# Kernel optimization log

Measured on AMD Instinct MI355X. Metric: run time of the kernel, lower is better.

## Reference

```python
import jax, jax.numpy as jnp
import numpy as np

EPS = 1e-08

def setup_inputs() -> dict:
    key = jax.random.key(0)
    kH, kF, kQ, kK, kV = jax.random.split(key, 5)
    B, N, d = 8192, 16, 512
    H = jax.random.normal(kH, (B, N, d), dtype=jnp.float32)
    F_raw = jax.random.uniform(kF, (B, N), dtype=jnp.float32)
    F = F_raw / jnp.sum(F_raw, axis=-1, keepdims=True)  # fractions sum to 1
    s = 1.0 / np.sqrt(d)
    W_Q = jax.random.normal(kQ, (d, d), dtype=jnp.float32) * s
    W_K = jax.random.normal(kK, (d, d), dtype=jnp.float32) * s
    W_V = jax.random.normal(kV, (d, d), dtype=jnp.float32) * s
    return {"H": H, "F": F, "W_Q": W_Q, "W_K": W_K, "W_V": W_V}

def reference(H, F, W_Q, W_K, W_V):
    d = H.shape[-1]
    scale = jnp.asarray(d, H.dtype) ** 0.5
    # nn.Linear(d, d, bias=False): y = x @ W.T
    Q = jnp.einsum('bnd,ed->bne', H, W_Q)
    K = jnp.einsum('bnd,ed->bne', H, W_K)
    V = jnp.einsum('bnd,ed->bne', H, W_V)
    scores = jnp.einsum('bqd,bkd->bqk', Q, K) / scale  # [B,N,N]
    scores = scores + jnp.log(F + EPS)[:, None, :]      # fraction bias over keys
    alpha = jax.nn.softmax(scores, axis=-1)
    h_attn = jnp.einsum('bqk,bkd->bqd', alpha, V)
    h_out = H + h_attn                                  # residual
    h_poly = jnp.einsum('bn,bnd->bd', F, h_out)         # fraction-weighted pool
    return h_poly
```

## Files before the change

### kernel.cpp

```cpp
#include <hip/hip_runtime.h>

typedef __bf16 bf16x8 __attribute__((ext_vector_type(8)));
typedef float f32x4 __attribute__((ext_vector_type(4)));

__device__ __forceinline__ unsigned short f2bf(float f) {
    unsigned int u = __builtin_bit_cast(unsigned int, f);
    u += 0x7fffu + ((u >> 16) & 1u);
    return (unsigned short)(u >> 16);
}
__device__ __forceinline__ float bf2f(unsigned short u) {
    return __builtin_bit_cast(float, (unsigned)u << 16);
}

__device__ __forceinline__ unsigned swz1k(unsigned byte) {
    return byte ^ ((byte >> 6) & 0x70u);
}

__device__ __forceinline__ void bar_lgkm() {
    asm volatile("s_waitcnt lgkmcnt(0)\n\ts_barrier" ::: "memory");
}
#define SB() __builtin_amdgcn_sched_barrier(0)

__global__ __launch_bounds__(256) void prep_kernel(
    const float* __restrict__ Wq, const float* __restrict__ Wk,
    const float* __restrict__ Wv, unsigned short* __restrict__ Pc,
    unsigned short* __restrict__ Wvb)
{
    int b = blockIdx.x;
    if (b < 1024) {
        int j0 = (b >> 4) * 8;
        int kc = b & 15;
        int jloc = threadIdx.x >> 5;
        int t = threadIdx.x & 31;
        int j = j0 + jloc, d = kc * 32 + t;
        float acc = 0.f;
        #pragma unroll 8
        for (int e = 0; e < 512; ++e)
            acc = fmaf(Wk[e * 512 + j], Wq[e * 512 + d], acc);
        Pc[((kc * 512) + j) * 32 + t] = f2bf(acc);
    } else {
        int i = (b - 1024) * 256 + (int)threadIdx.x;
        Wvb[i] = f2bf(Wv[i]);
    }
}

__device__ __forceinline__ void issue_q(int q, int tid, const float4* hsrc, float4 (&hq)[2]) {
    #pragma unroll
    for (int r = 0; r < 2; ++r) {
        int flat = r * 1024 + tid;
        hq[r] = hsrc[(flat >> 5) * 128 + q * 32 + (flat & 31)];
    }
}

__device__ __forceinline__ void convert_q(int q, int tid, char* HBF, float4 (&hq)[2]) {
    #pragma unroll
    for (int r = 0; r < 2; ++r) {
        int flat = r * 1024 + tid;
        int row = flat >> 5, ch = flat & 31;
        ushort4 bv;
        bv.x = f2bf(hq[r].x); bv.y = f2bf(hq[r].y);
        bv.z = f2bf(hq[r].z); bv.w = f2bf(hq[r].w);
        *(ushort4*)(HBF + swz1k((unsigned)row * 1024u + (unsigned)(q * 32 + ch) * 8u)) = bv;
    }
}

template<bool PREF>
__device__ __forceinline__ void gemm_q(
    int kcbase, int tid, int rl, int kg,
    const unsigned short* bptr, char* HBF,
    bf16x8 (&st0)[2], bf16x8 (&st1)[2],
    f32x4 (&acc)[4][2],
    float4 (&hq)[2], const float4* hsrc, int hq_q)
{
    #pragma unroll
    for (int k = 0; k < 4; ++k) {
        const int kc = kcbase + k;
        bf16x8 bn[2];
        if (kc + 2 < 16) {
            #pragma unroll
            for (int jj = 0; jj < 2; ++jj)
                bn[jj] = *(const bf16x8*)(bptr + (kc + 2) * 16384 + jj * 512);
        }
        if (PREF && k == 1) {
            SB();
            issue_q(hq_q, tid, hsrc, hq);
            SB();
        }
        bf16x8 a[4];
        #pragma unroll
        for (int i = 0; i < 4; ++i) {
            unsigned off = (unsigned)(i * 16 + rl) * 1024u + (unsigned)kc * 64u + (unsigned)kg * 16u;
            a[i] = *(bf16x8*)(HBF + swz1k(off));
        }
        #pragma unroll
        for (int i = 0; i < 4; ++i)
            #pragma unroll
            for (int jj = 0; jj < 2; ++jj)
                acc[i][jj] = __builtin_amdgcn_mfma_f32_16x16x32_bf16(a[i], st0[jj], acc[i][jj], 0, 0, 0);
        #pragma unroll
        for (int jj = 0; jj < 2; ++jj) { st0[jj] = st1[jj]; st1[jj] = bn[jj]; }
    }
}

__global__ __launch_bounds__(1024, 4) void attn_main_kernel(
    const float* __restrict__ H, const float* __restrict__ F,
    const unsigned short* __restrict__ Pc,
    float* __restrict__ out, unsigned short* __restrict__ g_ws)
{
    extern __shared__ char smem[];
    char* HBF  = smem;
    char* TBF  = smem + 65536;
    float* wbuf = (float*)(smem + 131072);
    float* FL   = (float*)(smem + 131328);
    float* LFL  = (float*)(smem + 131584);

    const int tid = threadIdx.x;
    const int wv = tid >> 6;
    const int ln = tid & 63;
    const int rl = ln & 15;
    const int kg = ln >> 4;
    const int blk = blockIdx.x;
    const long long gr0 = (long long)blk * 64;
    const float4* hsrc = (const float4*)(H + gr0 * 512);

    float fval = 0.f;
    if (tid < 64) fval = F[blk * 64 + tid];

    float4 hqA[2], hqB[2];
    issue_q(0, tid, hsrc, hqA);

    const unsigned short* bptr = Pc + ((wv * 32 + rl) * 32 + kg * 8);
    bf16x8 st0[2], st1[2];
    #pragma unroll
    for (int jj = 0; jj < 2; ++jj) st0[jj] = *(const bf16x8*)(bptr + 0 * 16384 + jj * 512);
    #pragma unroll
    for (int jj = 0; jj < 2; ++jj) st1[jj] = *(const bf16x8*)(bptr + 1 * 16384 + jj * 512);

    issue_q(1, tid, hsrc, hqB);

    if (tid < 64) {
        FL[tid] = fval;
        LFL[tid] = logf(fval + 1e-8f);
    }

    f32x4 acc[4][2];
    #pragma unroll
    for (int i = 0; i < 4; ++i)
        #pragma unroll
        for (int jj = 0; jj < 2; ++jj)
            acc[i][jj] = f32x4{0.f, 0.f, 0.f, 0.f};

    convert_q(0, tid, HBF, hqA);
    bar_lgkm();
    gemm_q<true >(0,  tid, rl, kg, bptr, HBF, st0, st1, acc, hqA, hsrc, 2);
    convert_q(1, tid, HBF, hqB);
    bar_lgkm();
    gemm_q<true >(4,  tid, rl, kg, bptr, HBF, st0, st1, acc, hqB, hsrc, 3);
    convert_q(2, tid, HBF, hqA);
    bar_lgkm();
    gemm_q<false>(8,  tid, rl, kg, bptr, HBF, st0, st1, acc, hqA, hsrc, 0);
    convert_q(3, tid, HBF, hqB);
    bar_lgkm();
    gemm_q<false>(12, tid, rl, kg, bptr, HBF, st0, st1, acc, hqB, hsrc, 0);

    #pragma unroll
    for (int i = 0; i < 4; ++i)
        #pragma unroll
        for (int jj = 0; jj < 2; ++jj)
            #pragma unroll
            for (int p = 0; p < 4; ++p) {
                unsigned row = (unsigned)(i * 16 + kg * 4 + p);
                unsigned col = (unsigned)(wv * 32 + jj * 16 + rl);
                *(unsigned short*)(TBF + swz1k(row * 1024u + col * 2u)) = f2bf(acc[i][jj][p]);
            }
    bar_lgkm();

    if (wv < 4) {
        f32x4 sc0 = f32x4{0.f,0.f,0.f,0.f}, sc1 = sc0, sc2 = sc0, sc3 = sc0;
        __builtin_amdgcn_s_setprio(1);
        #pragma unroll
        for (int kc = 0; kc < 16; ++kc) {
            unsigned off = (unsigned)(wv * 16 + rl) * 1024u + (unsigned)kc * 64u + (unsigned)kg * 16u;
            bf16x8 aT = *(bf16x8*)(TBF + swz1k(off));
            bf16x8 bH = *(bf16x8*)(HBF + swz1k(off));
            if ((kc & 3) == 0) sc0 = __builtin_amdgcn_mfma_f32_16x16x32_bf16(aT, bH, sc0, 0, 0, 0);
            else if ((kc & 3) == 1) sc1 = __builtin_amdgcn_mfma_f32_16x16x32_bf16(aT, bH, sc1, 0, 0, 0);
            else if ((kc & 3) == 2) sc2 = __builtin_amdgcn_mfma_f32_16x16x32_bf16(aT, bH, sc2, 0, 0, 0);
            else sc3 = __builtin_amdgcn_mfma_f32_16x16x32_bf16(aT, bH, sc3, 0, 0, 0);
        }
        __builtin_amdgcn_s_setprio(0);
        f32x4 sc;
        #pragma unroll
        for (int p = 0; p < 4; ++p) sc[p] = (sc0[p] + sc1[p]) + (sc2[p] + sc3[p]);

        float bias = LFL[wv * 16 + rl];
        float alpha[4];
        #pragma unroll
        for (int p = 0; p < 4; ++p) {
            float s = sc[p] * 0.044194173824159216f + bias;
            float m = s;
            m = fmaxf(m, __shfl_xor(m, 8));
            m = fmaxf(m, __shfl_xor(m, 4));
            m = fmaxf(m, __shfl_xor(m, 2));
            m = fmaxf(m, __shfl_xor(m, 1));
            float e = expf(s - m);
            float sum = e;
            sum += __shfl_xor(sum, 8);
            sum += __shfl_xor(sum, 4);
            sum += __shfl_xor(sum, 2);
            sum += __shfl_xor(sum, 1);
            alpha[p] = e / sum;
        }
        float part = 0.f;
        #pragma unroll
        for (int p = 0; p < 4; ++p) part += FL[wv * 16 + kg * 4 + p] * alpha[p];
        part += __shfl_xor(part, 16);
        part += __shfl_xor(part, 32);
        if (ln < 16) wbuf[wv * 16 + ln] = part;
    } else if (wv < 12) {
        int u = wv - 4;
        int bb = u >> 1, dh = u & 1;
        const long long Bg = (long long)blk * 4 + bb;
        int d0 = dh * 256 + ln * 4;
        float o[4];
        #pragma unroll
        for (int q = 0; q < 4; ++q) o[q] = 0.f;
        #pragma unroll
        for (int k = 0; k < 16; ++k) {
            unsigned off = (unsigned)(bb * 16 + k) * 1024u + (unsigned)d0 * 2u;
            ushort4 h = *(ushort4*)(HBF + swz1k(off));
            float fk = FL[bb * 16 + k];
            o[0] = fmaf(fk, bf2f(h.x), o[0]); o[1] = fmaf(fk, bf2f(h.y), o[1]);
            o[2] = fmaf(fk, bf2f(h.z), o[2]); o[3] = fmaf(fk, bf2f(h.w), o[3]);
        }
        float4 oa; oa.x = o[0]; oa.y = o[1]; oa.z = o[2]; oa.w = o[3];
        *(float4*)(out + Bg * 512 + d0) = oa;
    }
    bar_lgkm();

    {
        int bb = wv >> 2, q4 = wv & 3;
        const long long Bg = (long long)blk * 4 + bb;
        int d0 = q4 * 128 + ln * 2;
        float g0 = 0.f, g1 = 0.f;
        #pragma unroll
        for (int k = 0; k < 16; ++k) {
            unsigned off = (unsigned)(bb * 16 + k) * 1024u + (unsigned)d0 * 2u;
            ushort2 h = *(ushort2*)(HBF + swz1k(off));
            float wk = wbuf[bb * 16 + k];
            g0 = fmaf(wk, bf2f(h.x), g0); g1 = fmaf(wk, bf2f(h.y), g1);
        }
        ushort2 g2; g2.x = f2bf(g0); g2.y = f2bf(g1);
        *(ushort2*)(g_ws + Bg * 512 + d0) = g2;
    }
}

__global__ __launch_bounds__(512) void out_gemm_kernel(
    const unsigned short* __restrict__ g_ws,
    const unsigned short* __restrict__ Wvb,
    float* __restrict__ out)
{
    extern __shared__ char smem[];
    const int tid = threadIdx.x;
    const int wv = tid >> 6, ln = tid & 63;
    const int rl = ln & 15, kg = ln >> 4;
    const long long r0 = (long long)blockIdx.x * 32;
    {
        const uint4* src = (const uint4*)(g_ws + r0 * 512);
        #pragma unroll
        for (int q = 0; q < 4; ++q) {
            int idx = q * 512 + tid;
            *(uint4*)(smem + swz1k((unsigned)idx * 16u)) = src[idx];
        }
    }
    __syncthreads();
    f32x4 acc[2][4];
    #pragma unroll
    for (int i = 0; i < 2; ++i)
        #pragma unroll
        for (int jj = 0; jj < 4; ++jj)
            acc[i][jj] = f32x4{0.f, 0.f, 0.f, 0.f};
    for (int kc = 0; kc < 16; ++kc) {
        bf16x8 a[2];
        #pragma unroll
        for (int i = 0; i < 2; ++i) {
            unsigned off = (unsigned)(i * 16 + rl) * 1024u + (unsigned)kc * 64u + (unsigned)kg * 16u;
            a[i] = *(bf16x8*)(smem + swz1k(off));
        }
        bf16x8 bfr[4];
        #pragma unroll
        for (int jj = 0; jj < 4; ++jj) {
            int n = wv * 64 + jj * 16 + rl;
            bfr[jj] = *(const bf16x8*)(Wvb + n * 512 + kc * 32 + kg * 8);
        }
        #pragma unroll
        for (int i = 0; i < 2; ++i)
            #pragma unroll
            for (int jj = 0; jj < 4; ++jj)
                acc[i][jj] = __builtin_amdgcn_mfma_f32_16x16x32_bf16(a[i], bfr[jj], acc[i][jj], 0, 0, 0);
    }
    #pragma unroll
    for (int i = 0; i < 2; ++i)
        #pragma unroll
        for (int jj = 0; jj < 4; ++jj)
            #pragma unroll
            for (int p = 0; p < 4; ++p) {
                int row = i * 16 + kg * 4 + p;
                int col = wv * 64 + jj * 16 + rl;
                out[(r0 + row) * 512 + col] += acc[i][jj][p];
            }
}

extern "C" void kernel_launch(void* const* d_in, const int* in_sizes, int n_in,
                              void* d_out, int out_size, void* d_ws, size_t ws_size,
                              hipStream_t stream)
{
    const float* H  = (const float*)d_in[0];
    const float* F  = (const float*)d_in[1];
    const float* Wq = (const float*)d_in[2];
    const float* Wk = (const float*)d_in[3];
    const float* Wv = (const float*)d_in[4];
    float* out = (float*)d_out;

    unsigned short* Pc  = (unsigned short*)d_ws;
    unsigned short* Wvb = Pc + 262144;
    unsigned short* g   = Wvb + 262144;
    (void)in_sizes; (void)n_in; (void)out_size; (void)ws_size;

    prep_kernel<<<dim3(2048), dim3(256), 0, stream>>>(Wq, Wk, Wv, Pc, Wvb);
    attn_main_kernel<<<dim3(2048), dim3(1024), 131840, stream>>>(H, F, Pc, out, g);
    out_gemm_kernel<<<dim3(256), dim3(512), 32768, stream>>>(g, Wvb, out);
}
```

Measured before the change: 193.6 us.

## Compute Wq^T Wk weight product with bf16 MFMA tiles in prep kernel

After: 167.8 us. 13.3% less time.

```diff
diff --git a/kernel.cpp b/kernel.cpp
--- a/kernel.cpp
+++ b/kernel.cpp
@@ -26,21 +26,66 @@
     const float* __restrict__ Wv, unsigned short* __restrict__ Pc,
     unsigned short* __restrict__ Wvb)
 {
-    int b = blockIdx.x;
-    if (b < 1024) {
-        int j0 = (b >> 4) * 8;
-        int kc = b & 15;
-        int jloc = threadIdx.x >> 5;
-        int t = threadIdx.x & 31;
-        int j = j0 + jloc, d = kc * 32 + t;
-        float acc = 0.f;
+    const int b = blockIdx.x;
+    const int tid = threadIdx.x;
+    if (b >= 256) {
+        const float4* src = (const float4*)Wv;
         #pragma unroll 8
-        for (int e = 0; e < 512; ++e)
-            acc = fmaf(Wk[e * 512 + j], Wq[e * 512 + d], acc);
-        Pc[((kc * 512) + j) * 32 + t] = f2bf(acc);
-    } else {
-        int i = (b - 1024) * 256 + (int)threadIdx.x;
-        Wvb[i] = f2bf(Wv[i]);
+        for (int r = 0; r < 32; ++r) {
+            int fl = (b - 256) * 8192 + r * 256 + tid;
+            float4 v = src[fl];
+            ushort4 o;
+            o.x = f2bf(v.x); o.y = f2bf(v.y); o.z = f2bf(v.z); o.w = f2bf(v.w);
+            *(ushort4*)(Wvb + fl * 4) = o;
+        }
+        return;
+    }
+
+    extern __shared__ char smem[];
+    char* LDSA = smem;
+    char* LDSB = smem + 32768;
+
+    const int d0 = (b >> 4) * 32;
+    const int j0 = (b & 15) * 32;
+    const int wv = tid >> 6;
+    const int ln = tid & 63;
+    const int rl = ln & 15;
+    const int kg = ln >> 4;
+
+    {
+        const int c = tid >> 5;
+        const int el = tid & 31;
+        #pragma unroll
+        for (int p = 0; p < 16; ++p) {
+            const int e = p * 32 + el;
+            float4 qa = *(const float4*)(Wq + (long long)e * 512 + d0 + c * 4);
+            float4 qb = *(const float4*)(Wk + (long long)e * 512 + j0 + c * 4);
+            float av[4] = {qa.x, qa.y, qa.z, qa.w};
+            float bvv[4] = {qb.x, qb.y, qb.z, qb.w};
+            #pragma unroll
+            for (int k = 0; k < 4; ++k) {
+                unsigned byte = (unsigned)(c * 4 + k) * 1024u + (unsigned)e * 2u;
+                *(unsigned short*)(LDSA + swz1k(byte)) = f2bf(av[k]);
+                *(unsigned short*)(LDSB + swz1k(byte)) = f2bf(bvv[k]);
+            }
+        }
+    }
+    bar_lgkm();
+
+    const int df = wv >> 1, jf = wv & 1;
+    f32x4 acc = f32x4{0.f, 0.f, 0.f, 0.f};
+    #pragma unroll
+    for (int kc = 0; kc < 16; ++kc) {
+        unsigned cb = (unsigned)kc * 64u + (unsigned)kg * 16u;
+        bf16x8 a = *(bf16x8*)(LDSA + swz1k((unsigned)(df * 16 + rl) * 1024u + cb));
+        bf16x8 bb = *(bf16x8*)(LDSB + swz1k((unsigned)(jf * 16 + rl) * 1024u + cb));
+        acc = __builtin_amdgcn_mfma_f32_16x16x32_bf16(a, bb, acc, 0, 0, 0);
+    }
+    #pragma unroll
+    for (int p = 0; p < 4; ++p) {
+        int d = d0 + df * 16 + kg * 4 + p;
+        int j = j0 + jf * 16 + rl;
+        Pc[((d >> 5) * 512 + j) * 32 + (d & 31)] = f2bf(acc[p]);
     }
 }
 
@@ -327,7 +372,7 @@
     unsigned short* g   = Wvb + 262144;
     (void)in_sizes; (void)n_in; (void)out_size; (void)ws_size;
 
-    prep_kernel<<<dim3(2048), dim3(256), 0, stream>>>(Wq, Wk, Wv, Pc, Wvb);
+    prep_kernel<<<dim3(264), dim3(256), 65536, stream>>>(Wq, Wk, Wv, Pc, Wvb);
     attn_main_kernel<<<dim3(2048), dim3(1024), 131840, stream>>>(H, F, Pc, out, g);
     out_gemm_kernel<<<dim3(256), dim3(512), 32768, stream>>>(g, Wvb, out);
 }
```
